# Performance work log

Measured on AMD Instinct MI355X. Metric: run time of the kernel, lower is better.

Reference implementation:

```python
import jax, jax.numpy as jnp
import numpy as np

B, S1, S2 = 32, 60, 60
H, L, D = 100, 20, 300
V, CLS = 30000, 3


def _lstm(x, Wih, Whh, bih, bhh):
    # x: (B,T,Din); PyTorch gate order i,f,g,o
    xp = jnp.einsum('btd,gd->btg', x, Wih) + bih  # (B,T,4H)
    Hh = Whh.shape[1]
    init = (jnp.zeros((x.shape[0], Hh), x.dtype), jnp.zeros((x.shape[0], Hh), x.dtype))
    def step(carry, xt):
        hprev, cprev = carry
        g = xt + hprev @ Whh.T + bhh
        i, f, gg, o = jnp.split(g, 4, axis=-1)
        c = jax.nn.sigmoid(f) * cprev + jax.nn.sigmoid(i) * jnp.tanh(gg)
        hh = jax.nn.sigmoid(o) * jnp.tanh(c)
        return (hh, c), hh
    (hT, _), hs = jax.lax.scan(step, init, jnp.swapaxes(xp, 0, 1))
    return jnp.swapaxes(hs, 0, 1), hT


def _bilstm(x, pf, pb):
    hs_f, hT_f = _lstm(x, *pf)
    hs_b, hT_b = _lstm(x[:, ::-1], *pb)
    return hs_f, hs_b[:, ::-1], hT_f, hT_b


def _mp_single(v1, u, w):
    # cosine(w*v1_i, w*u) per perspective; v1 (B,S,H), u (B,H), w (H,L) -> (B,L,S)
    w2 = w * w
    n1 = jnp.sqrt(jnp.einsum('bih,hl->bil', v1 * v1, w2))
    nu = jnp.sqrt(jnp.einsum('bh,hl->bl', u * u, w2))
    num = jnp.einsum('bih,hl,bh->bil', v1, w2, u)
    return jnp.swapaxes(num / (n1 * nu[:, None, :]), 1, 2)


def _mp_pairwise(v1, v2, w):
    # full (B,L,S1,S2) multi-perspective cosine without materializing (B,L,S,H)
    w2 = w * w
    n1 = jnp.sqrt(jnp.einsum('bih,hl->bil', v1 * v1, w2))  # (B,S1,L)
    n2 = jnp.sqrt(jnp.einsum('bjh,hl->bjl', v2 * v2, w2))  # (B,S2,L)
    num = jnp.einsum('bih,hl,bjh->blij', v1, w2, v2)
    return num / (jnp.moveaxis(n1, 2, 1)[..., None] * jnp.moveaxis(n2, 2, 1)[:, :, None, :])


def _cos_attn(v1, v2):
    n1 = jnp.linalg.norm(v1, axis=2, keepdims=True)
    n2 = jnp.linalg.norm(v2, axis=2, keepdims=True)
    return jnp.einsum('bih,bjh->bij', v1, v2) / (n1 * jnp.swapaxes(n2, 1, 2))


def _match_dir(cp, ch, w_full, w_max, w_am, w_amax, last_idx):
    mv_p_full = _mp_single(cp, ch[:, last_idx], w_full)
    mv_h_full = _mp_single(ch, cp[:, last_idx], w_full)
    m = _mp_pairwise(cp, ch, w_max)
    mv_p_max = m.max(axis=3)
    mv_h_max = m.max(axis=2)
    a = _cos_attn(cp, ch)  # (B,S1,S2)
    mean_h = jnp.einsum('bij,bjh->bih', a, ch) / (a.sum(2, keepdims=True) + 1e-10)
    mean_p = jnp.einsum('bij,bih->bjh', a, cp) / (a.sum(1)[..., None] + 1e-10)
    max_h = (ch[:, None, :, :] * a[..., None]).max(axis=2)  # (B,S1,H)
    max_p = (cp[:, :, None, :] * a[..., None]).max(axis=1)  # (B,S2,H)
    # original code slices [:, :, :, 0] -> matches against v2 position 0
    mv_p_am = _mp_single(cp, mean_h[:, 0], w_am)
    mv_h_am = _mp_single(ch, mean_p[:, 0], w_am)
    mv_p_amax = _mp_single(cp, max_h[:, 0], w_amax)
    mv_h_amax = _mp_single(ch, max_p[:, 0], w_amax)
    return (mv_p_full, mv_p_max, mv_p_am, mv_p_amax), (mv_h_full, mv_h_max, mv_h_am, mv_h_amax)


def _forward(p_idx, h_idx, word_emb, ctxf, ctxb, ws, aggf, aggb, fc1_W, fc1_b, fc2_W, fc2_b):
    p = word_emb[p_idx]
    h = word_emb[h_idx]
    cpf, cpb, _, _ = _bilstm(p, ctxf, ctxb)
    chf, chb, _, _ = _bilstm(h, ctxf, ctxb)
    w1, w2, w3, w4, w5, w6, w7, w8 = ws
    pf, hf = _match_dir(cpf, chf, w1, w3, w5, w7, -1)
    pb, hb = _match_dir(cpb, chb, w2, w4, w6, w8, 0)
    mv_p = jnp.swapaxes(jnp.concatenate(pf + pb, axis=1), 1, 2)  # (B,S1,8L)
    mv_h = jnp.swapaxes(jnp.concatenate(hf + hb, axis=1), 1, 2)
    _, _, pTf, pTb = _bilstm(mv_p, aggf, aggb)
    _, _, hTf, hTb = _bilstm(mv_h, aggf, aggb)
    x = jnp.concatenate([pTf, pTb, hTf, hTb], axis=1)  # (B,4H)
    x = jnp.tanh(x @ fc1_W.T + fc1_b)
    return x @ fc2_W.T + fc2_b


def setup_inputs() -> dict:
    key = jax.random.key(0)
    ks = iter(jax.random.split(key, 48))
    def nrm(shape, s):
        return (jax.random.normal(next(ks), shape) * s).astype(jnp.float32)
    inp = {}
    inp['p'] = jax.random.randint(next(ks), (B, S1), 0, V)
    inp['h'] = jax.random.randint(next(ks), (B, S2), 0, V)
    inp['word_emb'] = nrm((V, D), 0.1)
    for pre, din in (('ctx', D), ('agg', 8 * L)):
        for d in ('f', 'b'):
            inp[pre + '_Wih_' + d] = nrm((4 * H, din), (2.0 / din) ** 0.5)
            inp[pre + '_Whh_' + d] = nrm((4 * H, H), (1.0 / H) ** 0.5)
            inp[pre + '_bih_' + d] = jnp.zeros((4 * H,), jnp.float32)
            inp[pre + '_bhh_' + d] = jnp.zeros((4 * H,), jnp.float32)
    for i in range(1, 9):
        inp['w' + str(i)] = nrm((H, L), (2.0 / H) ** 0.5)
    inp['fc1_W'] = nrm((2 * H, 4 * H), 0.005)
    inp['fc1_b'] = jnp.zeros((2 * H,), jnp.float32)
    inp['fc2_W'] = nrm((CLS, 2 * H), 0.005)
    inp['fc2_b'] = jnp.zeros((CLS,), jnp.float32)
    return inp


def reference(p, h, word_emb, ctx_Wih_f, ctx_Whh_f, ctx_bih_f, ctx_bhh_f, ctx_Wih_b, ctx_Whh_b, ctx_bih_b, ctx_bhh_b, w1, w2, w3, w4, w5, w6, w7, w8, agg_Wih_f, agg_Whh_f, agg_bih_f, agg_bhh_f, agg_Wih_b, agg_Whh_b, agg_bih_b, agg_bhh_b, fc1_W, fc1_b, fc2_W, fc2_b):
    return _forward(p, h, word_emb,
                    (ctx_Wih_f, ctx_Whh_f, ctx_bih_f, ctx_bhh_f),
                    (ctx_Wih_b, ctx_Whh_b, ctx_bih_b, ctx_bhh_b),
                    (w1, w2, w3, w4, w5, w6, w7, w8),
                    (agg_Wih_f, agg_Whh_f, agg_bih_f, agg_bhh_f),
                    (agg_Wih_b, agg_Whh_b, agg_bih_b, agg_bhh_b),
                    fc1_W, fc1_b, fc2_W, fc2_b)
```

## Files before the change

### kernel.cpp

```cpp
#include <hip/hip_runtime.h>
#include <math.h>

#define B_   32
#define T_   60
#define D_   300
#define HID  100
#define G4   400
#define L_   20

#define XP_OFF   0u
#define HSC_OFF  3072000u
#define HSA_OFF  3840000u
#define MV_OFF   4608000u
#define AV_OFF   5222400u

__global__ __launch_bounds__(256) void gemm_dual(
    const float* __restrict__ A0, const float* __restrict__ A1,
    const int* __restrict__ idx0, const int* __restrict__ idx1,
    const float* __restrict__ Wf, const float* __restrict__ Wb,
    const float* __restrict__ bf, const float* __restrict__ bb,
    float* __restrict__ C, int K)
{
    __shared__ float As[16][68];
    __shared__ float Bs[16][68];
    const int tid = threadIdx.x;
    const int m0 = blockIdx.y * 64;
    const int n0 = blockIdx.x * 64;
    const bool is_h = (m0 >= 1920);
    const float* __restrict__ Abase = is_h ? A1 : A0;
    const int* __restrict__ idx = is_h ? idx1 : idx0;
    const int mloc0 = m0 - (is_h ? 1920 : 0);

    const int r = tid >> 2;
    const int q = tid & 3;

    const int arow = mloc0 + r;
    const int srow = idx ? idx[arow] : arow;
    const float* __restrict__ Arow = Abase + (size_t)srow * K;
    const int n_my = n0 + r;
    const float* __restrict__ Wrow = (n_my < 400) ? (Wf + (size_t)n_my * K)
                      : ((n_my < 800) ? (Wb + (size_t)(n_my - 400) * K) : nullptr);

    const int tm = (tid >> 4) << 2;
    const int tn = (tid & 15) << 2;
    float acc[4][4] = {};
    for (int k0 = 0; k0 < K; k0 += 16) {
        const int k = k0 + q * 4;
        float4 av4 = make_float4(0.f, 0.f, 0.f, 0.f);
        float4 bv4 = make_float4(0.f, 0.f, 0.f, 0.f);
        if (k < K) av4 = *reinterpret_cast<const float4*>(Arow + k);
        if (Wrow != nullptr && k < K) bv4 = *reinterpret_cast<const float4*>(Wrow + k);
        __syncthreads();
        As[q * 4 + 0][r] = av4.x; As[q * 4 + 1][r] = av4.y;
        As[q * 4 + 2][r] = av4.z; As[q * 4 + 3][r] = av4.w;
        Bs[q * 4 + 0][r] = bv4.x; Bs[q * 4 + 1][r] = bv4.y;
        Bs[q * 4 + 2][r] = bv4.z; Bs[q * 4 + 3][r] = bv4.w;
        __syncthreads();
        #pragma unroll
        for (int kk = 0; kk < 16; ++kk) {
            const float4 a4 = *reinterpret_cast<const float4*>(&As[kk][tm]);
            const float4 b4 = *reinterpret_cast<const float4*>(&Bs[kk][tn]);
            const float a[4] = {a4.x, a4.y, a4.z, a4.w};
            const float b[4] = {b4.x, b4.y, b4.z, b4.w};
            #pragma unroll
            for (int i = 0; i < 4; i++)
                #pragma unroll
                for (int j = 0; j < 4; j++) acc[i][j] = fmaf(a[i], b[j], acc[i][j]);
        }
    }
    #pragma unroll
    for (int i = 0; i < 4; i++)
        #pragma unroll
        for (int j = 0; j < 4; j++) {
            const int n = n0 + tn + j;
            if (n < 800) {
                const int m = m0 + tm + i;
                const int s = (m >= 1920 ? 2 : 0) + (n >= 400 ? 1 : 0);
                const int ml = m - (m >= 1920 ? 1920 : 0);
                const int nl = n - (n >= 400 ? 400 : 0);
                const float bias = (n >= 400) ? bb[nl] : bf[nl];
                const int pos = (nl % 100) * 4 + nl / 100;
                C[((size_t)s * 1920 + ml) * 400 + pos] = acc[i][j] + bias;
            }
        }
}

__global__ __launch_bounds__(448, 1) void lstm_scan(
    const float* __restrict__ xp,
    const float* __restrict__ Whh_f, const float* __restrict__ Whh_b,
    const float* __restrict__ bhh_f, const float* __restrict__ bhh_b,
    float* __restrict__ hs)
{
    const int blk = blockIdx.x;
    const int s = blk >> 5, b = blk & 31;
    const int dir = s & 1;
    const float* __restrict__ Whh = dir ? Whh_b : Whh_f;
    const float* __restrict__ bhh = dir ? bhh_b : bhh_f;
    const int tid = threadIdx.x;
    const int g = tid & 3;
    const int j = tid >> 2;
    const bool act = tid < G4;

    __shared__ __align__(16) float h_lds[2][HID];

    float wreg[HID];
    float bias = 0.f;
    if (act) {
        const int row = g * HID + j;
        bias = bhh[row];
        #pragma unroll
        for (int k = 0; k < HID; ++k) wreg[k] = Whh[row * HID + k];
    }
    if (tid < HID) h_lds[0][tid] = 0.f;
    float c_reg = 0.f;

    const float* __restrict__ xp0 = xp + ((size_t)s * B_ + b) * T_ * G4;
    float* __restrict__ hs0 = hs + ((size_t)s * B_ + b) * T_ * HID;

    int t = dir ? (T_ - 1) : 0;
    const int tstep = dir ? -1 : 1;
    float xA = 0.f, xB = 0.f;
    if (act) {
        xA = xp0[(size_t)t * G4 + tid];
        xB = xp0[(size_t)(t + tstep) * G4 + tid];
    }
    int cur = 0;
    __syncthreads();

    for (int st = 0; st < T_; ++st) {
        if (act) {
            const float4* __restrict__ hp = reinterpret_cast<const float4*>(h_lds[cur]);
            float a0 = bias + xA, a1 = 0.f, a2 = 0.f, a3 = 0.f;
            #pragma unroll
            for (int k = 0; k < HID; k += 4) {
                const float4 h4 = hp[k >> 2];
                a0 = fmaf(h4.x, wreg[k + 0], a0);
                a1 = fmaf(h4.y, wreg[k + 1], a1);
                a2 = fmaf(h4.z, wreg[k + 2], a2);
                a3 = fmaf(h4.w, wreg[k + 3], a3);
            }
            xA = xB;
            if (st + 2 < T_) xB = xp0[(size_t)(t + 2 * tstep) * G4 + tid];
            const float acc = (a0 + a1) + (a2 + a3);
            const float z = (g == 2) ? (-2.f * acc) : (-acc);
            const float sig = 1.f / (1.f + expf(z));
            const float a = (g == 2) ? fmaf(2.f, sig, -1.f) : sig;
            const float v1 = __shfl_xor(a, 1);
            const float v2 = __shfl_xor(a, 2);
            const float v3 = __shfl_xor(v1, 2);
            if (g == 0) {
                c_reg = fmaf(v1, c_reg, a * v2);
                const float hv = v3 * tanhf(c_reg);
                h_lds[cur ^ 1][j] = hv;
                hs0[(size_t)t * HID + j] = hv;
            }
        }
        t += tstep;
        cur ^= 1;
        __syncthreads();
    }
}

__global__ __launch_bounds__(128) void attn_kernel(
    const float* __restrict__ hs_ctx, float* __restrict__ av)
{
    const int d = blockIdx.x >> 5;
    const int b = blockIdx.x & 31;
    const float* __restrict__ cp = hs_ctx + ((size_t)(0 + d) * B_ + b) * T_ * HID;
    const float* __restrict__ ch = hs_ctx + ((size_t)(2 + d) * B_ + b) * T_ * HID;
    const int tid = threadIdx.x;
    __shared__ float cp0[HID], ch0[HID];
    __shared__ float arow[T_], acol[T_];
    __shared__ float nrm[2], asum[2];
    if (tid < HID) { cp0[tid] = cp[tid]; ch0[tid] = ch[tid]; }
    __syncthreads();
    if (tid < 2) {
        const float* v = tid ? ch0 : cp0;
        float sum = 0.f;
        for (int h = 0; h < HID; h++) sum += v[h] * v[h];
        nrm[tid] = sqrtf(sum);
    }
    __syncthreads();
    if (tid < T_) {
        const float* r = ch + (size_t)tid * HID;
        float dot = 0.f, n2 = 0.f;
        for (int h = 0; h < HID; h++) { const float x = r[h]; dot += cp0[h] * x; n2 += x * x; }
        arow[tid] = dot / (nrm[0] * sqrtf(n2));
    } else if (tid >= 64 && tid < 64 + T_) {
        const int i = tid - 64;
        const float* r = cp + (size_t)i * HID;
        float dot = 0.f, n2 = 0.f;
        for (int h = 0; h < HID; h++) { const float x = r[h]; dot += x * ch0[h]; n2 += x * x; }
        acol[i] = dot / (sqrtf(n2) * nrm[1]);
    }
    __syncthreads();
    if (tid < 2) {
        const float* a = tid ? acol : arow;
        float sum = 0.f;
        for (int j = 0; j < T_; j++) sum += a[j];
        asum[tid] = sum;
    }
    __syncthreads();
    if (tid < HID) {
        float m = 0.f, mx = -INFINITY;
        for (int j = 0; j < T_; j++) {
            const float x = ch[(size_t)j * HID + tid] * arow[j];
            m += x; mx = fmaxf(mx, x);
        }
        av[((size_t)(d * 4 + 0) * B_ + b) * HID + tid] = m / (asum[0] + 1e-10f);
        av[((size_t)(d * 4 + 1) * B_ + b) * HID + tid] = mx;
        float m2 = 0.f, mx2 = -INFINITY;
        for (int i = 0; i < T_; i++) {
            const float x = cp[(size_t)i * HID + tid] * acol[i];
            m2 += x; mx2 = fmaxf(mx2, x);
        }
        av[((size_t)(d * 4 + 2) * B_ + b) * HID + tid] = m2 / (asum[1] + 1e-10f);
        av[((size_t)(d * 4 + 3) * B_ + b) * HID + tid] = mx2;
    }
}

struct MPCfg {
    const float* v1;
    const float* u;
    int ustride;
    const float* w;
    float* outp;
    int choff;
};
struct MPCfgs { MPCfg c[12]; };

__global__ __launch_bounds__(256) void mp_single_kernel(MPCfgs cfgs)
{
    const int ci = blockIdx.x >> 5;
    const int b = blockIdx.x & 31;
    const MPCfg cfg = cfgs.c[ci];
    const int tid = threadIdx.x;
    __shared__ float w2[HID][L_];
    __shared__ float uw[HID][L_];
    __shared__ float u_l[HID];
    __shared__ float nul[L_];
    if (tid < HID) u_l[tid] = cfg.u[(size_t)b * cfg.ustride + tid];
    for (int e = tid; e < HID * L_; e += 256) {
        const float wv = cfg.w[e];
        w2[e / L_][e % L_] = wv * wv;
    }
    __syncthreads();
    for (int e = tid; e < HID * L_; e += 256) uw[e / L_][e % L_] = w2[e / L_][e % L_] * u_l[e / L_];
    if (tid < L_) {
        float sum = 0.f;
        for (int h = 0; h < HID; h++) sum += u_l[h] * u_l[h] * w2[h][tid];
        nul[tid] = sqrtf(sum);
    }
    __syncthreads();
    const float* __restrict__ v1b = cfg.v1 + (size_t)b * T_ * HID;
    for (int p = tid; p < T_ * L_; p += 256) {
        const int i = p / L_, l = p % L_;
        const float* __restrict__ v = v1b + (size_t)i * HID;
        float num = 0.f, den = 0.f;
        for (int h = 0; h < HID; h++) {
            const float x = v[h];
            num = fmaf(x, uw[h][l], num);
            den = fmaf(x * x, w2[h][l], den);
        }
        cfg.outp[((size_t)b * T_ + i) * 160 + cfg.choff + l] = num / (sqrtf(den) * nul[l]);
    }
}

__global__ __launch_bounds__(256) void mp_pair_kernel(
    const float* __restrict__ hs_ctx, const float* __restrict__ w3,
    const float* __restrict__ w4, float* __restrict__ mv_p, float* __restrict__ mv_h)
{
    const int x = blockIdx.x;
    const int l = x % L_;
    const int b = (x / L_) & 31;
    const int d = x / (L_ * B_);
    const float* __restrict__ cp = hs_ctx + ((size_t)(0 + d) * B_ + b) * T_ * HID;
    const float* __restrict__ ch = hs_ctx + ((size_t)(2 + d) * B_ + b) * T_ * HID;
    const float* __restrict__ w = d ? w4 : w3;
    const int tid = threadIdx.x;

    __shared__ __align__(16) float Ut[HID][T_];
    __shared__ __align__(16) float Vt[HID][T_];
    __shared__ float aw[HID];
    __shared__ float rn1[T_], rn2[T_];
    float* pmi = &Ut[0][0];
    float* pmj = &Ut[0][0] + 60 * 17 + 4;

    if (tid < HID) aw[tid] = fabsf(w[tid * L_ + l]);
    __syncthreads();
    for (int e = tid; e < T_ * HID; e += 256) {
        const int i = e / HID, h = e % HID;
        const float a = aw[h];
        Ut[h][i] = cp[e] * a;
        Vt[h][i] = ch[e] * a;
    }
    __syncthreads();
    if (tid < T_) {
        float s = 0.f;
        for (int h = 0; h < HID; h++) { const float v = Ut[h][tid]; s = fmaf(v, v, s); }
        rn1[tid] = 1.0f / sqrtf(s);
    } else if (tid >= 64 && tid < 64 + T_) {
        const int j = tid - 64;
        float s = 0.f;
        for (int h = 0; h < HID; h++) { const float v = Vt[h][j]; s = fmaf(v, v, s); }
        rn2[j] = 1.0f / sqrtf(s);
    }
    __syncthreads();

    float rmax[4], cmax[4];
    int i0 = 0, j0 = 0, ti = 0, tj = 0;
    if (tid < 225) {
        tj = tid % 15;
        ti = tid / 15;
        i0 = tj * 4; j0 = ti * 4;
        float acc[4][4] = {};
        #pragma unroll 4
        for (int h = 0; h < HID; ++h) {
            const float4 u = *reinterpret_cast<const float4*>(&Ut[h][i0]);
            const float4 v = *reinterpret_cast<const float4*>(&Vt[h][j0]);
            const float uu[4] = {u.x, u.y, u.z, u.w};
            const float vv[4] = {v.x, v.y, v.z, v.w};
            #pragma unroll
            for (int r2 = 0; r2 < 4; r2++)
                #pragma unroll
                for (int s2 = 0; s2 < 4; s2++) acc[r2][s2] = fmaf(uu[r2], vv[s2], acc[r2][s2]);
        }
        const float r1[4] = {rn1[i0], rn1[i0 + 1], rn1[i0 + 2], rn1[i0 + 3]};
        const float r2v[4] = {rn2[j0], rn2[j0 + 1], rn2[j0 + 2], rn2[j0 + 3]};
        #pragma unroll
        for (int r2 = 0; r2 < 4; r2++) { rmax[r2] = -INFINITY; }
        #pragma unroll
        for (int s2 = 0; s2 < 4; s2++) { cmax[s2] = -INFINITY; }
        #pragma unroll
        for (int r2 = 0; r2 < 4; r2++)
            #pragma unroll
            for (int s2 = 0; s2 < 4; s2++) {
                const float val = acc[r2][s2] * (r1[r2] * r2v[s2]);
                rmax[r2] = fmaxf(rmax[r2], val);
                cmax[s2] = fmaxf(cmax[s2], val);
            }
    }
    __syncthreads();
    if (tid < 225) {
        #pragma unroll
        for (int r2 = 0; r2 < 4; r2++) pmi[(i0 + r2) * 17 + ti] = rmax[r2];
        #pragma unroll
        for (int s2 = 0; s2 < 4; s2++) pmj[tj * 61 + (j0 + s2)] = cmax[s2];
    }
    __syncthreads();
    if (tid < T_) {
        float mx = -INFINITY;
        for (int q = 0; q < 15; q++) mx = fmaxf(mx, pmi[tid * 17 + q]);
        mv_p[((size_t)b * T_ + tid) * 160 + d * 80 + 20 + l] = mx;
    } else if (tid >= 64 && tid < 64 + T_) {
        const int j = tid - 64;
        float mx = -INFINITY;
        for (int q = 0; q < 15; q++) mx = fmaxf(mx, pmj[q * 61 + j]);
        mv_h[((size_t)b * T_ + j) * 160 + d * 80 + 20 + l] = mx;
    }
}

__global__ __launch_bounds__(256) void fc_final(
    const float* __restrict__ hs_agg, const float* __restrict__ fc1W,
    const float* __restrict__ fc1b, const float* __restrict__ fc2W,
    const float* __restrict__ fc2b, float* __restrict__ out)
{
    const int b = blockIdx.x;
    const int tid = threadIdx.x;
    __shared__ float x[400];
    __shared__ float y[200];
    if (tid < HID) {
        x[tid]           = hs_agg[((size_t)(0 * B_ + b) * T_ + 59) * HID + tid];
        x[HID + tid]     = hs_agg[((size_t)(1 * B_ + b) * T_ + 0) * HID + tid];
        x[2 * HID + tid] = hs_agg[((size_t)(2 * B_ + b) * T_ + 59) * HID + tid];
        x[3 * HID + tid] = hs_agg[((size_t)(3 * B_ + b) * T_ + 0) * HID + tid];
    }
    __syncthreads();
    if (tid < 200) {
        float s = fc1b[tid];
        const float* __restrict__ wr = fc1W + (size_t)tid * 400;
        for (int k = 0; k < 400; k++) s = fmaf(x[k], wr[k], s);
        y[tid] = tanhf(s);
    }
    __syncthreads();
    if (tid < 3) {
        float s = fc2b[tid];
        const float* __restrict__ wr = fc2W + (size_t)tid * 200;
        for (int k = 0; k < 200; k++) s = fmaf(y[k], wr[k], s);
        out[b * 3 + tid] = s;
    }
}

extern "C" void kernel_launch(void* const* d_in, const int* in_sizes, int n_in,
                              void* d_out, int out_size, void* d_ws, size_t ws_size,
                              hipStream_t stream) {
    const int* p_idx = (const int*)d_in[0];
    const int* h_idx = (const int*)d_in[1];
    const float* emb = (const float*)d_in[2];
    const float* ctx_Wih_f = (const float*)d_in[3];
    const float* ctx_Whh_f = (const float*)d_in[4];
    const float* ctx_bih_f = (const float*)d_in[5];
    const float* ctx_bhh_f = (const float*)d_in[6];
    const float* ctx_Wih_b = (const float*)d_in[7];
    const float* ctx_Whh_b = (const float*)d_in[8];
    const float* ctx_bih_b = (const float*)d_in[9];
    const float* ctx_bhh_b = (const float*)d_in[10];
    const float* agg_Wih_f = (const float*)d_in[11];
    const float* agg_Whh_f = (const float*)d_in[12];
    const float* agg_bih_f = (const float*)d_in[13];
    const float* agg_bhh_f = (const float*)d_in[14];
    const float* agg_Wih_b = (const float*)d_in[15];
    const float* agg_Whh_b = (const float*)d_in[16];
    const float* agg_bih_b = (const float*)d_in[17];
    const float* agg_bhh_b = (const float*)d_in[18];
    const float* w1 = (const float*)d_in[19];
    const float* w2 = (const float*)d_in[20];
    const float* w3 = (const float*)d_in[21];
    const float* w4 = (const float*)d_in[22];
    const float* w5 = (const float*)d_in[23];
    const float* w6 = (const float*)d_in[24];
    const float* w7 = (const float*)d_in[25];
    const float* w8 = (const float*)d_in[26];
    const float* fc1W = (const float*)d_in[27];
    const float* fc1b = (const float*)d_in[28];
    const float* fc2W = (const float*)d_in[29];
    const float* fc2b = (const float*)d_in[30];

    float* ws = (float*)d_ws;
    float* xp = ws + XP_OFF;
    float* hsc = ws + HSC_OFF;
    float* hsa = ws + HSA_OFF;
    float* mvp = ws + MV_OFF;
    float* mvh = mvp + (size_t)B_ * T_ * 160;
    float* av = ws + AV_OFF;

    const dim3 ggrid(13, 60);

    gemm_dual<<<ggrid, 256, 0, stream>>>(emb, emb, p_idx, h_idx,
                                         ctx_Wih_f, ctx_Wih_b, ctx_bih_f, ctx_bih_b, xp, 300);

    lstm_scan<<<128, 448, 0, stream>>>(xp, ctx_Whh_f, ctx_Whh_b, ctx_bhh_f, ctx_bhh_b, hsc);

    attn_kernel<<<64, 128, 0, stream>>>(hsc, av);

    MPCfgs cfgs;
    for (int d = 0; d < 2; d++) {
        const float* cp_d = hsc + (size_t)(0 + d) * B_ * T_ * HID;
        const float* ch_d = hsc + (size_t)(2 + d) * B_ * T_ * HID;
        const int last = d ? 0 : (T_ - 1);
        const float* wfull = d ? w2 : w1;
        const float* wam = d ? w6 : w5;
        const float* wamax = d ? w8 : w7;
        float* avp0 = av + (size_t)(d * 4 + 0) * B_ * HID;
        float* avp1 = av + (size_t)(d * 4 + 1) * B_ * HID;
        float* avp2 = av + (size_t)(d * 4 + 2) * B_ * HID;
        float* avp3 = av + (size_t)(d * 4 + 3) * B_ * HID;
        cfgs.c[d * 6 + 0] = {cp_d, ch_d + last * HID, T_ * HID, wfull, mvp, d * 80 + 0};
        cfgs.c[d * 6 + 1] = {cp_d, avp0, HID, wam, mvp, d * 80 + 40};
        cfgs.c[d * 6 + 2] = {cp_d, avp1, HID, wamax, mvp, d * 80 + 60};
        cfgs.c[d * 6 + 3] = {ch_d, cp_d + last * HID, T_ * HID, wfull, mvh, d * 80 + 0};
        cfgs.c[d * 6 + 4] = {ch_d, avp2, HID, wam, mvh, d * 80 + 40};
        cfgs.c[d * 6 + 5] = {ch_d, avp3, HID, wamax, mvh, d * 80 + 60};
    }
    mp_single_kernel<<<384, 256, 0, stream>>>(cfgs);
    mp_pair_kernel<<<1280, 256, 0, stream>>>(hsc, w3, w4, mvp, mvh);

    gemm_dual<<<ggrid, 256, 0, stream>>>(mvp, mvh, nullptr, nullptr,
                                         agg_Wih_f, agg_Wih_b, agg_bih_f, agg_bih_b, xp, 160);

    lstm_scan<<<128, 448, 0, stream>>>(xp, agg_Whh_f, agg_Whh_b, agg_bhh_f, agg_bhh_b, hsa);

    fc_final<<<32, 256, 0, stream>>>(hsa, fc1W, fc1b, fc2W, fc2b, (float*)d_out);
}
```

Before: 380.7 us.

## Restructure LSTM scan to two gates per thread with readlane h broadcast

Result: slower. 497.8 us (+30.8%).

```diff
diff --git a/kernel.cpp b/kernel.cpp
--- a/kernel.cpp
+++ b/kernel.cpp
@@ -38,8 +38,10 @@
     const int srow = idx ? idx[arow] : arow;
     const float* __restrict__ Arow = Abase + (size_t)srow * K;
     const int n_my = n0 + r;
-    const float* __restrict__ Wrow = (n_my < 400) ? (Wf + (size_t)n_my * K)
-                      : ((n_my < 800) ? (Wb + (size_t)(n_my - 400) * K) : nullptr);
+    const int nl_my = (n_my < 400) ? n_my : n_my - 400;
+    const int wsrc_my = (nl_my & 3) * 100 + (nl_my >> 2);
+    const float* __restrict__ Wrow = (n_my < 400) ? (Wf + (size_t)wsrc_my * K)
+                      : ((n_my < 800) ? (Wb + (size_t)wsrc_my * K) : nullptr);
 
     const int tm = (tid >> 4) << 2;
     const int tn = (tid & 15) << 2;
@@ -78,14 +80,14 @@
                 const int s = (m >= 1920 ? 2 : 0) + (n >= 400 ? 1 : 0);
                 const int ml = m - (m >= 1920 ? 1920 : 0);
                 const int nl = n - (n >= 400 ? 400 : 0);
-                const float bias = (n >= 400) ? bb[nl] : bf[nl];
-                const int pos = (nl % 100) * 4 + nl / 100;
-                C[((size_t)s * 1920 + ml) * 400 + pos] = acc[i][j] + bias;
+                const int wsrc = (nl & 3) * 100 + (nl >> 2);
+                const float bias = (n >= 400) ? bb[wsrc] : bf[wsrc];
+                C[((size_t)s * 1920 + ml) * 400 + nl] = acc[i][j] + bias;
             }
         }
 }
 
-__global__ __launch_bounds__(448, 1) void lstm_scan(
+__global__ __launch_bounds__(256, 1) void lstm_scan(
     const float* __restrict__ xp,
     const float* __restrict__ Whh_f, const float* __restrict__ Whh_b,
     const float* __restrict__ bhh_f, const float* __restrict__ bhh_b,
@@ -97,63 +99,87 @@
     const float* __restrict__ Whh = dir ? Whh_b : Whh_f;
     const float* __restrict__ bhh = dir ? bhh_b : bhh_f;
     const int tid = threadIdx.x;
-    const int g = tid & 3;
-    const int j = tid >> 2;
-    const bool act = tid < G4;
+    const int p = tid & 1;
+    const int j = tid >> 1;
+    const bool act = tid < 200;
+    const int jj = act ? j : 99;
 
     __shared__ __align__(16) float h_lds[2][HID];
 
-    float wreg[HID];
-    float bias = 0.f;
-    if (act) {
-        const int row = g * HID + j;
-        bias = bhh[row];
-        #pragma unroll
-        for (int k = 0; k < HID; ++k) wreg[k] = Whh[row * HID + k];
-    }
+    float wa[HID], wb[HID];
+    {
+        const int ra = (p ? 2 : 0) * HID + jj;
+        const int rb = (p ? 3 : 1) * HID + jj;
+        #pragma unroll
+        for (int k = 0; k < HID; ++k) {
+            wa[k] = Whh[(size_t)ra * HID + k];
+            wb[k] = Whh[(size_t)rb * HID + k];
+        }
+    }
+    const float ba  = bhh[(p ? 2 : 0) * HID + jj];
+    const float bb2 = bhh[(p ? 3 : 1) * HID + jj];
+
     if (tid < HID) h_lds[0][tid] = 0.f;
     float c_reg = 0.f;
 
-    const float* __restrict__ xp0 = xp + ((size_t)s * B_ + b) * T_ * G4;
+    const float2* __restrict__ xp2 =
+        reinterpret_cast<const float2*>(xp + ((size_t)s * B_ + b) * T_ * G4);
     float* __restrict__ hs0 = hs + ((size_t)s * B_ + b) * T_ * HID;
 
     int t = dir ? (T_ - 1) : 0;
     const int tstep = dir ? -1 : 1;
-    float xA = 0.f, xB = 0.f;
+    float2 xA = make_float2(0.f, 0.f), xB = xA;
     if (act) {
-        xA = xp0[(size_t)t * G4 + tid];
-        xB = xp0[(size_t)(t + tstep) * G4 + tid];
+        xA = xp2[(size_t)t * 200 + tid];
+        xB = xp2[(size_t)(t + tstep) * 200 + tid];
     }
     int cur = 0;
     __syncthreads();
 
     for (int st = 0; st < T_; ++st) {
-        if (act) {
-            const float4* __restrict__ hp = reinterpret_cast<const float4*>(h_lds[cur]);
-            float a0 = bias + xA, a1 = 0.f, a2 = 0.f, a3 = 0.f;
-            #pragma unroll
-            for (int k = 0; k < HID; k += 4) {
-                const float4 h4 = hp[k >> 2];
-                a0 = fmaf(h4.x, wreg[k + 0], a0);
-                a1 = fmaf(h4.y, wreg[k + 1], a1);
-                a2 = fmaf(h4.z, wreg[k + 2], a2);
-                a3 = fmaf(h4.w, wreg[k + 3], a3);
-            }
-            xA = xB;
-            if (st + 2 < T_) xB = xp0[(size_t)(t + 2 * tstep) * G4 + tid];
-            const float acc = (a0 + a1) + (a2 + a3);
-            const float z = (g == 2) ? (-2.f * acc) : (-acc);
-            const float sig = 1.f / (1.f + expf(z));
-            const float a = (g == 2) ? fmaf(2.f, sig, -1.f) : sig;
-            const float v1 = __shfl_xor(a, 1);
-            const float v2 = __shfl_xor(a, 2);
-            const float v3 = __shfl_xor(v1, 2);
-            if (g == 0) {
-                c_reg = fmaf(v1, c_reg, a * v2);
-                const float hv = v3 * tanhf(c_reg);
-                h_lds[cur ^ 1][j] = hv;
-                hs0[(size_t)t * HID + j] = hv;
-            }
+        const int lane = tid & 63;
+        float4 hq = make_float4(0.f, 0.f, 0.f, 0.f);
+        if (lane < 25) hq = *reinterpret_cast<const float4*>(&h_lds[cur][lane * 4]);
+
+        float aa = ba + xA.x, ab = bb2 + xA.y;
+        float aa2 = 0.f, ab2 = 0.f;
+        #pragma unroll
+        for (int c = 0; c < 25; ++c) {
+            const float h0 = __int_as_float(__builtin_amdgcn_readlane(__float_as_int(hq.x), c));
+            const float h1 = __int_as_float(__builtin_amdgcn_readlane(__float_as_int(hq.y), c));
+            const float h2 = __int_as_float(__builtin_amdgcn_readlane(__float_as_int(hq.z), c));
+            const float h3 = __int_as_float(__builtin_amdgcn_readlane(__float_as_int(hq.w), c));
+            aa  = fmaf(h0, wa[4 * c + 0], aa);
+            aa2 = fmaf(h1, wa[4 * c + 1], aa2);
+            aa  = fmaf(h2, wa[4 * c + 2], aa);
+            aa2 = fmaf(h3, wa[4 * c + 3], aa2);
+            ab  = fmaf(h0, wb[4 * c + 0], ab);
+            ab2 = fmaf(h1, wb[4 * c + 1], ab2);
+            ab  = fmaf(h2, wb[4 * c + 2], ab);
+            ab2 = fmaf(h3, wb[4 * c + 3], ab2);
+        }
+        const float A  = aa + aa2;
+        const float Bv = ab + ab2;
+
+        xA = xB;
+        if (act && st + 2 < T_) xB = xp2[(size_t)(t + 2 * tstep) * 200 + tid];
+
+        float ra_, rb_;
+        if (p) {
+            ra_ = fmaf(2.f, 1.f / (1.f + expf(-2.f * A)), -1.f);
+            rb_ = 1.f / (1.f + expf(-Bv));
+        } else {
+            ra_ = 1.f / (1.f + expf(-A));
+            rb_ = 1.f / (1.f + expf(-Bv));
+        }
+        const float qa = __shfl_xor(ra_, 1);
+        const float qb = __shfl_xor(rb_, 1);
+        if (act && p == 0) {
+            c_reg = fmaf(rb_, c_reg, ra_ * qa);
+            const float th = fmaf(2.f, 1.f / (1.f + expf(-2.f * c_reg)), -1.f);
+            const float hv = qb * th;
+            h_lds[cur ^ 1][j] = hv;
+            hs0[(size_t)t * HID + j] = hv;
         }
         t += tstep;
         cur ^= 1;
@@ -253,8 +279,8 @@
     }
     __syncthreads();
     const float* __restrict__ v1b = cfg.v1 + (size_t)b * T_ * HID;
-    for (int p = tid; p < T_ * L_; p += 256) {
-        const int i = p / L_, l = p % L_;
+    for (int pp = tid; pp < T_ * L_; pp += 256) {
+        const int i = pp / L_, l = pp % L_;
         const float* __restrict__ v = v1b + (size_t)i * HID;
         float num = 0.f, den = 0.f;
         for (int h = 0; h < HID; h++) {
@@ -439,7 +465,7 @@
     gemm_dual<<<ggrid, 256, 0, stream>>>(emb, emb, p_idx, h_idx,
                                          ctx_Wih_f, ctx_Wih_b, ctx_bih_f, ctx_bih_b, xp, 300);
 
-    lstm_scan<<<128, 448, 0, stream>>>(xp, ctx_Whh_f, ctx_Whh_b, ctx_bhh_f, ctx_bhh_b, hsc);
+    lstm_scan<<<128, 256, 0, stream>>>(xp, ctx_Whh_f, ctx_Whh_b, ctx_bhh_f, ctx_bhh_b, hsc);
 
     attn_kernel<<<64, 128, 0, stream>>>(hsc, av);
 
@@ -468,7 +494,7 @@
     gemm_dual<<<ggrid, 256, 0, stream>>>(mvp, mvh, nullptr, nullptr,
                                          agg_Wih_f, agg_Wih_b, agg_bih_f, agg_bih_b, xp, 160);
 
-    lstm_scan<<<128, 448, 0, stream>>>(xp, agg_Whh_f, agg_Whh_b, agg_bhh_f, agg_bhh_b, hsa);
+    lstm_scan<<<128, 256, 0, stream>>>(xp, agg_Whh_f, agg_Whh_b, agg_bhh_f, agg_bhh_b, hsa);
 
     fc_final<<<32, 256, 0, stream>>>(hsa, fc1W, fc1b, fc2W, fc2b, (float*)d_out);
 }
```

## Broadcast LSTM hidden state via scalar loads from global scratch instead of LDS

Applied to the files above, without the earlier changes.

Measured after the change: 488.8 us. +28.4%, slower.

```diff
diff --git a/kernel.cpp b/kernel.cpp
--- a/kernel.cpp
+++ b/kernel.cpp
@@ -13,6 +13,9 @@
 #define HSA_OFF  3840000u
 #define MV_OFF   4608000u
 #define AV_OFF   5222400u
+#define HX_OFF   5248000u
+
+typedef __attribute__((ext_vector_type(4))) int i4x;
 
 __global__ __launch_bounds__(256) void gemm_dual(
     const float* __restrict__ A0, const float* __restrict__ A1,
@@ -38,8 +41,10 @@
     const int srow = idx ? idx[arow] : arow;
     const float* __restrict__ Arow = Abase + (size_t)srow * K;
     const int n_my = n0 + r;
-    const float* __restrict__ Wrow = (n_my < 400) ? (Wf + (size_t)n_my * K)
-                      : ((n_my < 800) ? (Wb + (size_t)(n_my - 400) * K) : nullptr);
+    const int nl_my = (n_my < 400) ? n_my : n_my - 400;
+    const int wsrc_my = (nl_my & 3) * 100 + (nl_my >> 2);
+    const float* __restrict__ Wrow = (n_my < 400) ? (Wf + (size_t)wsrc_my * K)
+                      : ((n_my < 800) ? (Wb + (size_t)wsrc_my * K) : nullptr);
 
     const int tm = (tid >> 4) << 2;
     const int tn = (tid & 15) << 2;
@@ -78,18 +83,24 @@
                 const int s = (m >= 1920 ? 2 : 0) + (n >= 400 ? 1 : 0);
                 const int ml = m - (m >= 1920 ? 1920 : 0);
                 const int nl = n - (n >= 400 ? 400 : 0);
-                const float bias = (n >= 400) ? bb[nl] : bf[nl];
-                const int pos = (nl % 100) * 4 + nl / 100;
-                C[((size_t)s * 1920 + ml) * 400 + pos] = acc[i][j] + bias;
+                const int wsrc = (nl & 3) * 100 + (nl >> 2);
+                const float bias = (n >= 400) ? bb[wsrc] : bf[wsrc];
+                C[((size_t)s * 1920 + ml) * 400 + nl] = acc[i][j] + bias;
             }
         }
 }
+
+#define FMA4(hv, wb) \
+    ac0 = fmaf(__int_as_float(hv.x), wreg[(wb) + 0], ac0); \
+    ac1 = fmaf(__int_as_float(hv.y), wreg[(wb) + 1], ac1); \
+    ac2 = fmaf(__int_as_float(hv.z), wreg[(wb) + 2], ac2); \
+    ac3 = fmaf(__int_as_float(hv.w), wreg[(wb) + 3], ac3);
 
 __global__ __launch_bounds__(448, 1) void lstm_scan(
     const float* __restrict__ xp,
     const float* __restrict__ Whh_f, const float* __restrict__ Whh_b,
     const float* __restrict__ bhh_f, const float* __restrict__ bhh_b,
-    float* __restrict__ hs)
+    float* __restrict__ hs, float* __restrict__ hx)
 {
     const int blk = blockIdx.x;
     const int s = blk >> 5, b = blk & 31;
@@ -101,21 +112,19 @@
     const int j = tid >> 2;
     const bool act = tid < G4;
 
-    __shared__ __align__(16) float h_lds[2][HID];
-
     float wreg[HID];
     float bias = 0.f;
     if (act) {
         const int row = g * HID + j;
         bias = bhh[row];
         #pragma unroll
-        for (int k = 0; k < HID; ++k) wreg[k] = Whh[row * HID + k];
-    }
-    if (tid < HID) h_lds[0][tid] = 0.f;
+        for (int k = 0; k < HID; ++k) wreg[k] = Whh[(size_t)row * HID + k];
+    }
     float c_reg = 0.f;
 
     const float* __restrict__ xp0 = xp + ((size_t)s * B_ + b) * T_ * G4;
     float* __restrict__ hs0 = hs + ((size_t)s * B_ + b) * T_ * HID;
+    float* __restrict__ hxr = hx + (size_t)blk * T_ * 128;
 
     int t = dir ? (T_ - 1) : 0;
     const int tstep = dir ? -1 : 1;
@@ -124,40 +133,87 @@
         xA = xp0[(size_t)t * G4 + tid];
         xB = xp0[(size_t)(t + tstep) * G4 + tid];
     }
-    int cur = 0;
+    i4x h00, h01, h02, h03, h04, h05, h06, h07;
+    i4x h08, h09, h10, h11, h12, h13, h14, h15;
+    const float* hp = hxr;
     __syncthreads();
 
     for (int st = 0; st < T_; ++st) {
-        if (act) {
-            const float4* __restrict__ hp = reinterpret_cast<const float4*>(h_lds[cur]);
-            float a0 = bias + xA, a1 = 0.f, a2 = 0.f, a3 = 0.f;
-            #pragma unroll
-            for (int k = 0; k < HID; k += 4) {
-                const float4 h4 = hp[k >> 2];
-                a0 = fmaf(h4.x, wreg[k + 0], a0);
-                a1 = fmaf(h4.y, wreg[k + 1], a1);
-                a2 = fmaf(h4.z, wreg[k + 2], a2);
-                a3 = fmaf(h4.w, wreg[k + 3], a3);
-            }
-            xA = xB;
-            if (st + 2 < T_) xB = xp0[(size_t)(t + 2 * tstep) * G4 + tid];
-            const float acc = (a0 + a1) + (a2 + a3);
-            const float z = (g == 2) ? (-2.f * acc) : (-acc);
-            const float sig = 1.f / (1.f + expf(z));
-            const float a = (g == 2) ? fmaf(2.f, sig, -1.f) : sig;
-            const float v1 = __shfl_xor(a, 1);
-            const float v2 = __shfl_xor(a, 2);
-            const float v3 = __shfl_xor(v1, 2);
-            if (g == 0) {
-                c_reg = fmaf(v1, c_reg, a * v2);
-                const float hv = v3 * tanhf(c_reg);
-                h_lds[cur ^ 1][j] = hv;
-                hs0[(size_t)t * HID + j] = hv;
-            }
-        }
+        float ac0 = bias + xA, ac1 = 0.f, ac2 = 0.f, ac3 = 0.f;
+        xA = xB;
+        if (st > 0) {
+            asm volatile("s_waitcnt lgkmcnt(0)"
+                : "+s"(h00), "+s"(h01), "+s"(h02), "+s"(h03),
+                  "+s"(h04), "+s"(h05), "+s"(h06), "+s"(h07),
+                  "+s"(h08), "+s"(h09), "+s"(h10), "+s"(h11),
+                  "+s"(h12), "+s"(h13), "+s"(h14), "+s"(h15));
+            FMA4(h00, 0)  FMA4(h01, 4)  FMA4(h02, 8)  FMA4(h03, 12)
+            FMA4(h04, 16) FMA4(h05, 20) FMA4(h06, 24) FMA4(h07, 28)
+            FMA4(h08, 32) FMA4(h09, 36) FMA4(h10, 40) FMA4(h11, 44)
+            FMA4(h12, 48) FMA4(h13, 52) FMA4(h14, 56) FMA4(h15, 60)
+            asm volatile(
+                "s_load_dwordx4 %0, %9, 256\n\t"
+                "s_load_dwordx4 %1, %9, 272\n\t"
+                "s_load_dwordx4 %2, %9, 288\n\t"
+                "s_load_dwordx4 %3, %9, 304\n\t"
+                "s_load_dwordx4 %4, %9, 320\n\t"
+                "s_load_dwordx4 %5, %9, 336\n\t"
+                "s_load_dwordx4 %6, %9, 352\n\t"
+                "s_load_dwordx4 %7, %9, 368\n\t"
+                "s_load_dwordx4 %8, %9, 384"
+                : "+s"(h00), "+s"(h01), "+s"(h02), "+s"(h03), "+s"(h04),
+                  "+s"(h05), "+s"(h06), "+s"(h07), "+s"(h08)
+                : "s"(hp));
+            asm volatile("s_waitcnt lgkmcnt(0)"
+                : "+s"(h00), "+s"(h01), "+s"(h02), "+s"(h03), "+s"(h04),
+                  "+s"(h05), "+s"(h06), "+s"(h07), "+s"(h08));
+            FMA4(h00, 64) FMA4(h01, 68) FMA4(h02, 72) FMA4(h03, 76)
+            FMA4(h04, 80) FMA4(h05, 84) FMA4(h06, 88) FMA4(h07, 92)
+            FMA4(h08, 96)
+        }
+        const float acc = (ac0 + ac1) + (ac2 + ac3);
+        const float z = (g == 2) ? (-2.f * acc) : (-acc);
+        const float sig = 1.f / (1.f + expf(z));
+        const float a = (g == 2) ? fmaf(2.f, sig, -1.f) : sig;
+        const float v1 = __shfl_xor(a, 1);
+        const float v2 = __shfl_xor(a, 2);
+        const float v3 = __shfl_xor(v1, 2);
+        float hv = 0.f;
+        if (act && g == 0) {
+            c_reg = fmaf(v1, c_reg, a * v2);
+            hv = v3 * fmaf(2.f, 1.f / (1.f + expf(-2.f * c_reg)), -1.f);
+            hxr[st * 128 + j] = hv;
+        }
+        asm volatile("" ::: "memory");
+        if (act && g == 0) hs0[(size_t)t * HID + j] = hv;
+        asm volatile("" ::: "memory");
+        if (act && st + 2 < T_) xB = xp0[(size_t)(t + 2 * tstep) * G4 + tid];
+        asm volatile("s_waitcnt vmcnt(1)" ::: "memory");
+        __syncthreads();
+        hp = hxr + st * 128;
+        asm volatile(
+            "s_load_dwordx4 %0,  %16, 0\n\t"
+            "s_load_dwordx4 %1,  %16, 16\n\t"
+            "s_load_dwordx4 %2,  %16, 32\n\t"
+            "s_load_dwordx4 %3,  %16, 48\n\t"
+            "s_load_dwordx4 %4,  %16, 64\n\t"
+            "s_load_dwordx4 %5,  %16, 80\n\t"
+            "s_load_dwordx4 %6,  %16, 96\n\t"
+            "s_load_dwordx4 %7,  %16, 112\n\t"
+            "s_load_dwordx4 %8,  %16, 128\n\t"
+            "s_load_dwordx4 %9,  %16, 144\n\t"
+            "s_load_dwordx4 %10, %16, 160\n\t"
+            "s_load_dwordx4 %11, %16, 176\n\t"
+            "s_load_dwordx4 %12, %16, 192\n\t"
+            "s_load_dwordx4 %13, %16, 208\n\t"
+            "s_load_dwordx4 %14, %16, 224\n\t"
+            "s_load_dwordx4 %15, %16, 240"
+            : "=s"(h00), "=s"(h01), "=s"(h02), "=s"(h03),
+              "=s"(h04), "=s"(h05), "=s"(h06), "=s"(h07),
+              "=s"(h08), "=s"(h09), "=s"(h10), "=s"(h11),
+              "=s"(h12), "=s"(h13), "=s"(h14), "=s"(h15)
+            : "s"(hp));
         t += tstep;
-        cur ^= 1;
-        __syncthreads();
     }
 }
 
@@ -253,8 +309,8 @@
     }
     __syncthreads();
     const float* __restrict__ v1b = cfg.v1 + (size_t)b * T_ * HID;
-    for (int p = tid; p < T_ * L_; p += 256) {
-        const int i = p / L_, l = p % L_;
+    for (int pp = tid; pp < T_ * L_; pp += 256) {
+        const int i = pp / L_, l = pp % L_;
         const float* __restrict__ v = v1b + (size_t)i * HID;
         float num = 0.f, den = 0.f;
         for (int h = 0; h < HID; h++) {
@@ -433,13 +489,14 @@
     float* mvp = ws + MV_OFF;
     float* mvh = mvp + (size_t)B_ * T_ * 160;
     float* av = ws + AV_OFF;
+    float* hx = ws + HX_OFF;
 
     const dim3 ggrid(13, 60);
 
     gemm_dual<<<ggrid, 256, 0, stream>>>(emb, emb, p_idx, h_idx,
                                          ctx_Wih_f, ctx_Wih_b, ctx_bih_f, ctx_bih_b, xp, 300);
 
-    lstm_scan<<<128, 448, 0, stream>>>(xp, ctx_Whh_f, ctx_Whh_b, ctx_bhh_f, ctx_bhh_b, hsc);
+    lstm_scan<<<128, 448, 0, stream>>>(xp, ctx_Whh_f, ctx_Whh_b, ctx_bhh_f, ctx_bhh_b, hsc, hx);
 
     attn_kernel<<<64, 128, 0, stream>>>(hsc, av);
 
@@ -468,7 +525,7 @@
     gemm_dual<<<ggrid, 256, 0, stream>>>(mvp, mvh, nullptr, nullptr,
                                          agg_Wih_f, agg_Wih_b, agg_bih_f, agg_bih_b, xp, 160);
 
-    lstm_scan<<<128, 448, 0, stream>>>(xp, agg_Whh_f, agg_Whh_b, agg_bhh_f, agg_bhh_b, hsa);
+    lstm_scan<<<128, 448, 0, stream>>>(xp, agg_Whh_f, agg_Whh_b, agg_bhh_f, agg_bhh_b, hsa, hx);
 
     fc_final<<<32, 256, 0, stream>>>(hsa, fc1W, fc1b, fc2W, fc2b, (float*)d_out);
 }
```
